# Kernel tuning notes

Hardware: AMD Instinct MI355X
Metric: run time of the kernel (lower is better)

Reference implementation:

```python
import jax, jax.numpy as jnp
import numpy as np

OUT_SIZE = 7          # pooled output resolution
SR = 2                # sampling_ratio (samples per bin side)
SCALES = (0.25, 0.125, 0.0625, 0.03125)   # FPN P2..P5 -> min_level=2, max_level=5
MIN_LEVEL, MAX_LEVEL = 2, 5
CANON_SIZE, CANON_LEVEL = 224.0, 4.0


def _roi_align(feat, boxes, bidx, scale):
    """ROIAlignV2 (aligned=True), fixed sampling_ratio.
    feat: [N,C,H,W]; boxes: [M,4] (x1,y1,x2,y2 in image coords); bidx: [M] int.
    Returns [M,C,OUT_SIZE,OUT_SIZE]."""
    N, C, H, W = feat.shape
    featT = jnp.transpose(feat, (0, 2, 3, 1))  # [N,H,W,C] for channel-last gathers
    # aligned=True: half-pixel offset
    x1 = boxes[:, 0] * scale - 0.5
    y1 = boxes[:, 1] * scale - 0.5
    x2 = boxes[:, 2] * scale - 0.5
    y2 = boxes[:, 3] * scale - 0.5
    bw = (x2 - x1) / OUT_SIZE
    bh = (y2 - y1) / OUT_SIZE
    # flattened per-bin sample offsets: for bin i, sample j -> i + (j+0.5)/SR
    k = jnp.arange(OUT_SIZE * SR)
    off = (k // SR).astype(feat.dtype) + ((k % SR).astype(feat.dtype) + 0.5) / SR  # [P]
    ys = y1[:, None] + off[None, :] * bh[:, None]  # [M,P]
    xs = x1[:, None] + off[None, :] * bw[:, None]  # [M,P]
    # validity (torchvision semantics: zero outside [-1, size])
    vy = (ys >= -1.0) & (ys <= H)
    vx = (xs >= -1.0) & (xs <= W)
    valid = vy[:, :, None] & vx[:, None, :]        # [M,P,P]
    y = jnp.clip(ys, 0.0, H - 1.0)
    x = jnp.clip(xs, 0.0, W - 1.0)
    y0 = jnp.floor(y).astype(jnp.int32)
    x0 = jnp.floor(x).astype(jnp.int32)
    y1i = jnp.minimum(y0 + 1, H - 1)
    x1i = jnp.minimum(x0 + 1, W - 1)
    ly = y - y0.astype(y.dtype)
    lx = x - x0.astype(x.dtype)
    hy, hx = 1.0 - ly, 1.0 - lx

    def gather(yi, xi):  # -> [M,P,P,C]
        return featT[bidx[:, None, None], yi[:, :, None], xi[:, None, :]]

    val = (hy[:, :, None] * hx[:, None, :])[..., None] * gather(y0, x0)
    val = val + (hy[:, :, None] * lx[:, None, :])[..., None] * gather(y0, x1i)
    val = val + (ly[:, :, None] * hx[:, None, :])[..., None] * gather(y1i, x0)
    val = val + (ly[:, :, None] * lx[:, None, :])[..., None] * gather(y1i, x1i)
    val = jnp.where(valid[..., None], val, 0.0)
    M = boxes.shape[0]
    # average SRxSR samples per bin
    val = val.reshape(M, OUT_SIZE, SR, OUT_SIZE, SR, C).mean(axis=(2, 4))
    return jnp.transpose(val, (0, 3, 1, 2))  # [M,C,7,7]


def _pool(feats, boxes):
    N, R, _ = boxes.shape
    b = boxes.reshape(-1, 4)                        # [M,4], M = N*R (pooler-format concat)
    bidx = jnp.repeat(jnp.arange(N), R)             # batch index column
    # assign_boxes_to_levels: log2 area bucketing
    sizes = jnp.sqrt(jnp.maximum((b[:, 2] - b[:, 0]) * (b[:, 3] - b[:, 1]), 0.0))
    lvl = jnp.floor(CANON_LEVEL + jnp.log2(sizes / CANON_SIZE + 1e-8))
    lvl = jnp.clip(lvl, MIN_LEVEL, MAX_LEVEL).astype(jnp.int32) - MIN_LEVEL  # [M] in [0,3]
    out = jnp.zeros((b.shape[0], feats[0].shape[1], OUT_SIZE, OUT_SIZE), feats[0].dtype)
    for l, (f, s) in enumerate(zip(feats, SCALES)):
        pooled = _roi_align(f, b, bidx, s)
        out = out + jnp.where((lvl == l)[:, None, None, None], pooled, 0.0)
    return out


def setup_inputs() -> dict:
    key = jax.random.key(0)
    ks = jax.random.split(key, 6)
    N, R, IMG = 2, 512, 1024.0
    shapes = [(2, 256, 256, 256), (2, 256, 128, 128), (2, 256, 64, 64), (2, 256, 32, 32)]
    feats = [jax.random.normal(ks[i], s, dtype=jnp.float32) for i, s in enumerate(shapes)]
    # box sizes log-uniform in [32, 800] px so all 4 levels get boxes
    wh = jnp.exp(jax.random.uniform(ks[4], (N, R, 2), minval=jnp.log(32.0), maxval=jnp.log(800.0)))
    cxy = jax.random.uniform(ks[5], (N, R, 2), minval=0.0, maxval=IMG)
    x1y1 = jnp.clip(cxy - wh / 2, 0.0, IMG)
    x2y2 = jnp.clip(cxy + wh / 2, 0.0, IMG)
    boxes = jnp.concatenate([x1y1, x2y2], axis=-1)  # [N,R,4]
    return {"feat0": feats[0], "feat1": feats[1], "feat2": feats[2], "feat3": feats[3], "boxes": boxes}


def reference(feat0, feat1, feat2, feat3, boxes):
    return _pool((feat0, feat1, feat2, feat3), boxes)
```

## Files before the change

kernel.cpp:

```cpp
#include <hip/hip_runtime.h>

#define OUT 7
#define CCH 256

__device__ __forceinline__ unsigned short f2bf(float f) {
    union { float f; unsigned int u; } v; v.f = f;
    unsigned int r = (v.u + 0x7FFFu + ((v.u >> 16) & 1u)) >> 16;
    return (unsigned short)r;
}
__device__ __forceinline__ float bf2f(unsigned short h) {
    union { unsigned int u; float f; } v; v.u = ((unsigned int)h) << 16;
    return v.f;
}

__global__ __launch_bounds__(256) void roi_pool_naive(
    const float* __restrict__ f0, const float* __restrict__ f1,
    const float* __restrict__ f2, const float* __restrict__ f3,
    const float* __restrict__ boxes, float* __restrict__ out,
    int M, int R)
{
    int idx = blockIdx.x * blockDim.x + threadIdx.x;
    int total = M * CCH * OUT * OUT;
    if (idx >= total) return;
    int pw = idx % OUT;
    int ph = (idx / OUT) % OUT;
    int c  = (idx / (OUT * OUT)) % CCH;
    int m  = idx / (OUT * OUT * CCH);
    int n  = m / R;
    const float bx1 = boxes[m * 4 + 0], by1 = boxes[m * 4 + 1];
    const float bx2 = boxes[m * 4 + 2], by2 = boxes[m * 4 + 3];
    float sz  = sqrtf(fmaxf((bx2 - bx1) * (by2 - by1), 0.0f));
    int lvl = (int)floorf(4.0f + log2f(sz / 224.0f + 1e-8f));
    lvl = min(max(lvl, 2), 5) - 2;
    const float* feat; int H, W; float scale;
    switch (lvl) {
        case 0:  feat = f0; H = 256; W = 256; scale = 0.25f;    break;
        case 1:  feat = f1; H = 128; W = 128; scale = 0.125f;   break;
        case 2:  feat = f2; H = 64;  W = 64;  scale = 0.0625f;  break;
        default: feat = f3; H = 32;  W = 32;  scale = 0.03125f; break;
    }
    const float* fp = feat + (size_t)(n * CCH + c) * (size_t)(H * W);
    float x1 = bx1 * scale - 0.5f, y1 = by1 * scale - 0.5f;
    float x2 = bx2 * scale - 0.5f, y2 = by2 * scale - 0.5f;
    float bw = (x2 - x1) * (1.0f / OUT), bh = (y2 - y1) * (1.0f / OUT);
    float acc = 0.0f;
    #pragma unroll
    for (int iy = 0; iy < 2; iy++) {
        float ys = y1 + ((float)ph + ((float)iy + 0.5f) * 0.5f) * bh;
        bool vy = (ys >= -1.0f) && (ys <= (float)H);
        float y = fminf(fmaxf(ys, 0.0f), (float)(H - 1));
        int y0 = (int)y;
        int y1i = min(y0 + 1, H - 1);
        float ly = y - (float)y0, hy = 1.0f - ly;
        #pragma unroll
        for (int ix = 0; ix < 2; ix++) {
            float xs = x1 + ((float)pw + ((float)ix + 0.5f) * 0.5f) * bw;
            bool vx = (xs >= -1.0f) && (xs <= (float)W);
            float x = fminf(fmaxf(xs, 0.0f), (float)(W - 1));
            int x0 = (int)x;
            int x1ii = min(x0 + 1, W - 1);
            float lx = x - (float)x0, hx = 1.0f - lx;
            if (vy && vx) {
                acc += hy * hx * fp[y0 * W + x0]  + hy * lx * fp[y0 * W + x1ii]
                     + ly * hx * fp[y1i * W + x0] + ly * lx * fp[y1i * W + x1ii];
            }
        }
    }
    out[idx] = acc * 0.25f;
}

__global__ __launch_bounds__(256) void transpose_bf16(
    const float* __restrict__ in, unsigned short* __restrict__ outp, int HW)
{
    __shared__ float tile[64][65];
    int hw0 = blockIdx.x * 64;
    int c0  = blockIdx.y * 64;
    int n   = blockIdx.z;
    int tx = threadIdx.x;
    int ty = threadIdx.y;

    const float4* in4 = (const float4*)(in + (size_t)n * CCH * HW);
    #pragma unroll
    for (int j = 0; j < 4; j++) {
        int c = c0 + ty + 16 * j;
        float4 v = in4[((size_t)c * HW + hw0) / 4 + tx];
        tile[ty + 16 * j][4 * tx + 0] = v.x;
        tile[ty + 16 * j][4 * tx + 1] = v.y;
        tile[ty + 16 * j][4 * tx + 2] = v.z;
        tile[ty + 16 * j][4 * tx + 3] = v.w;
    }
    __syncthreads();
    unsigned short* ob = outp + (size_t)n * HW * CCH;
    #pragma unroll
    for (int j = 0; j < 4; j++) {
        int hw = hw0 + ty + 16 * j;
        ushort4 u;
        u.x = f2bf(tile[4 * tx + 0][ty + 16 * j]);
        u.y = f2bf(tile[4 * tx + 1][ty + 16 * j]);
        u.z = f2bf(tile[4 * tx + 2][ty + 16 * j]);
        u.w = f2bf(tile[4 * tx + 3][ty + 16 * j]);
        ((ushort4*)(ob + (size_t)hw * CCH + c0))[tx] = u;
    }
}

__global__ __launch_bounds__(256) void roi_pool_cl(
    const unsigned short* __restrict__ t0, const unsigned short* __restrict__ t1,
    const unsigned short* __restrict__ t2, const unsigned short* __restrict__ t3,
    const float* __restrict__ boxes, float* __restrict__ out, int M, int R)
{
    int bx = blockIdx.x;
    int m, ph;
    if ((M & 7) == 0) {
        int q = bx / 56, rem = bx - q * 56;
        ph = rem >> 3;
        m  = q * 8 + (rem & 7);
    } else {
        m = bx / OUT; ph = bx % OUT;
    }
    int t = threadIdx.x;
    int n = m / R;

    const float bx1 = boxes[m * 4 + 0], by1 = boxes[m * 4 + 1];
    const float bx2 = boxes[m * 4 + 2], by2 = boxes[m * 4 + 3];
    float sz  = sqrtf(fmaxf((bx2 - bx1) * (by2 - by1), 0.0f));
    int lvl = (int)floorf(4.0f + log2f(sz / 224.0f + 1e-8f));
    lvl = min(max(lvl, 2), 5) - 2;

    const unsigned short* feat; int H, W; float scale;
    switch (lvl) {
        case 0:  feat = t0; H = 256; W = 256; scale = 0.25f;    break;
        case 1:  feat = t1; H = 128; W = 128; scale = 0.125f;   break;
        case 2:  feat = t2; H = 64;  W = 64;  scale = 0.0625f;  break;
        default: feat = t3; H = 32;  W = 32;  scale = 0.03125f; break;
    }
    const unsigned short* fb = feat + (size_t)n * H * W * CCH;

    float x1 = bx1 * scale - 0.5f, y1 = by1 * scale - 0.5f;
    float x2 = bx2 * scale - 0.5f, y2 = by2 * scale - 0.5f;
    float bw = (x2 - x1) * (1.0f / OUT), bh = (y2 - y1) * (1.0f / OUT);

    int   r0[2], r1[2];
    float lyv[2], hyv[2];
    bool  vyv[2];
    #pragma unroll
    for (int iy = 0; iy < 2; iy++) {
        float ys = y1 + ((float)ph + ((float)iy + 0.5f) * 0.5f) * bh;
        vyv[iy] = (ys >= -1.0f) && (ys <= (float)H);
        float y = fminf(fmaxf(ys, 0.0f), (float)(H - 1));
        int y0 = (int)y;
        int y1i = min(y0 + 1, H - 1);
        lyv[iy] = y - (float)y0;
        hyv[iy] = 1.0f - lyv[iy];
        r0[iy] = y0 * W * CCH;
        r1[iy] = y1i * W * CCH;
    }

    float acc[OUT];
    #pragma unroll
    for (int pw = 0; pw < OUT; pw++) {
        float a = 0.0f;
        #pragma unroll
        for (int ix = 0; ix < 2; ix++) {
            float xs = x1 + ((float)pw + ((float)ix + 0.5f) * 0.5f) * bw;
            bool vx = (xs >= -1.0f) && (xs <= (float)W);
            float x = fminf(fmaxf(xs, 0.0f), (float)(W - 1));
            int x0 = (int)x;
            int x1i = min(x0 + 1, W - 1);
            float lx = x - (float)x0;
            float hx = 1.0f - lx;
            int c0o = x0 * CCH;
            int c1o = x1i * CCH;
            #pragma unroll
            for (int iy = 0; iy < 2; iy++) {
                if (vyv[iy] && vx) {
                    const unsigned short* p00 = fb + __builtin_amdgcn_readfirstlane(r0[iy] + c0o);
                    const unsigned short* p01 = fb + __builtin_amdgcn_readfirstlane(r0[iy] + c1o);
                    const unsigned short* p10 = fb + __builtin_amdgcn_readfirstlane(r1[iy] + c0o);
                    const unsigned short* p11 = fb + __builtin_amdgcn_readfirstlane(r1[iy] + c1o);
                    float v00 = bf2f(p00[t]), v01 = bf2f(p01[t]);
                    float v10 = bf2f(p10[t]), v11 = bf2f(p11[t]);
                    a += hyv[iy] * (hx * v00 + lx * v01)
                       + lyv[iy] * (hx * v10 + lx * v11);
                }
            }
        }
        acc[pw] = a * 0.25f;
    }

    float* ob = out + (size_t)m * (CCH * OUT * OUT) + (size_t)t * (OUT * OUT) + ph * OUT;
    #pragma unroll
    for (int k = 0; k < OUT; k++) ob[k] = acc[k];
}

extern "C" void kernel_launch(void* const* d_in, const int* in_sizes, int n_in,
                              void* d_out, int out_size, void* d_ws, size_t ws_size,
                              hipStream_t stream) {
    const float* f0    = (const float*)d_in[0];
    const float* f1    = (const float*)d_in[1];
    const float* f2    = (const float*)d_in[2];
    const float* f3    = (const float*)d_in[3];
    const float* boxes = (const float*)d_in[4];
    float* out = (float*)d_out;

    int N = in_sizes[0] / (CCH * 256 * 256);
    int M = in_sizes[4] / 4;
    int R = M / N;

    size_t nshorts = (size_t)N * CCH * (65536 + 16384 + 4096 + 1024);
    if (ws_size >= nshorts * sizeof(unsigned short)) {
        unsigned short* t0 = (unsigned short*)d_ws;
        unsigned short* t1 = t0 + (size_t)N * CCH * 65536;
        unsigned short* t2 = t1 + (size_t)N * CCH * 16384;
        unsigned short* t3 = t2 + (size_t)N * CCH * 4096;
        dim3 blk(16, 16);
        transpose_bf16<<<dim3(65536 / 64, CCH / 64, N), blk, 0, stream>>>(f0, t0, 65536);
        transpose_bf16<<<dim3(16384 / 64, CCH / 64, N), blk, 0, stream>>>(f1, t1, 16384);
        transpose_bf16<<<dim3(4096  / 64, CCH / 64, N), blk, 0, stream>>>(f2, t2, 4096);
        transpose_bf16<<<dim3(1024  / 64, CCH / 64, N), blk, 0, stream>>>(f3, t3, 1024);
        roi_pool_cl<<<M * OUT, 256, 0, stream>>>(t0, t1, t2, t3, boxes, out, M, R);
    } else {
        int total = M * CCH * OUT * OUT;
        roi_pool_naive<<<(total + 255) / 256, 256, 0, stream>>>(f0, f1, f2, f3, boxes, out, M, R);
    }
}
```

Before: 312.3 us.

## Merge per-level transposes into one launch and pool one box per block

Combines the four per-level channel-last bf16 transpose kernels into a single launch that decodes level, channel tile and batch from a flat block index. The pooling kernel now assigns one block per box and loops over all seven output rows, instead of one block per box row. This cuts launch overhead and repeated per-box setup, but reduces the pooling grid sevenfold, which lowers parallelism and latency hiding.

Result: slower. 386.5 us (+23.8%).

```diff
diff --git a/kernel.cpp b/kernel.cpp
--- a/kernel.cpp
+++ b/kernel.cpp
@@ -69,15 +69,35 @@
     out[idx] = acc * 0.25f;
 }
 
-__global__ __launch_bounds__(256) void transpose_bf16(
-    const float* __restrict__ in, unsigned short* __restrict__ outp, int HW)
+__global__ __launch_bounds__(256) void transpose_all(
+    const float* __restrict__ f0, const float* __restrict__ f1,
+    const float* __restrict__ f2, const float* __restrict__ f3,
+    unsigned short* __restrict__ o0, unsigned short* __restrict__ o1,
+    unsigned short* __restrict__ o2, unsigned short* __restrict__ o3,
+    int N)
 {
     __shared__ float tile[64][65];
-    int hw0 = blockIdx.x * 64;
-    int c0  = blockIdx.y * 64;
-    int n   = blockIdx.z;
-    int tx = threadIdx.x;
-    int ty = threadIdx.y;
+
+    int rem = blockIdx.x;
+    const int nb0 = 4096 * N;
+    const int nb1 = 1024 * N;
+    const int nb2 = 256 * N;
+    const float* in; unsigned short* op; int HW, lshift;
+    if (rem < nb0)        { in = f0; op = o0; HW = 65536; lshift = 10; }
+    else { rem -= nb0;
+      if (rem < nb1)      { in = f1; op = o1; HW = 16384; lshift = 8;  }
+      else { rem -= nb1;
+        if (rem < nb2)    { in = f2; op = o2; HW = 4096;  lshift = 6;  }
+        else { rem -= nb2;  in = f3; op = o3; HW = 1024;  lshift = 4;  }
+      }
+    }
+    int hw0 = (rem & ((1 << lshift) - 1)) << 6;
+    int c0  = ((rem >> lshift) & 3) << 6;
+    int n   = rem >> (lshift + 2);
+
+    int tid = threadIdx.x;
+    int tx = tid & 15;
+    int ty = tid >> 4;
 
     const float4* in4 = (const float4*)(in + (size_t)n * CCH * HW);
     #pragma unroll
@@ -90,7 +110,7 @@
         tile[ty + 16 * j][4 * tx + 3] = v.w;
     }
     __syncthreads();
-    unsigned short* ob = outp + (size_t)n * HW * CCH;
+    unsigned short* ob = op + (size_t)n * HW * CCH;
     #pragma unroll
     for (int j = 0; j < 4; j++) {
         int hw = hw0 + ty + 16 * j;
@@ -103,20 +123,12 @@
     }
 }
 
-__global__ __launch_bounds__(256) void roi_pool_cl(
+__global__ __launch_bounds__(256) void roi_pool_box(
     const unsigned short* __restrict__ t0, const unsigned short* __restrict__ t1,
     const unsigned short* __restrict__ t2, const unsigned short* __restrict__ t3,
     const float* __restrict__ boxes, float* __restrict__ out, int M, int R)
 {
-    int bx = blockIdx.x;
-    int m, ph;
-    if ((M & 7) == 0) {
-        int q = bx / 56, rem = bx - q * 56;
-        ph = rem >> 3;
-        m  = q * 8 + (rem & 7);
-    } else {
-        m = bx / OUT; ph = bx % OUT;
-    }
+    int m = blockIdx.x;
     int t = threadIdx.x;
     int n = m / R;
 
@@ -139,57 +151,61 @@
     float x2 = bx2 * scale - 0.5f, y2 = by2 * scale - 0.5f;
     float bw = (x2 - x1) * (1.0f / OUT), bh = (y2 - y1) * (1.0f / OUT);
 
-    int   r0[2], r1[2];
-    float lyv[2], hyv[2];
-    bool  vyv[2];
-    #pragma unroll
-    for (int iy = 0; iy < 2; iy++) {
-        float ys = y1 + ((float)ph + ((float)iy + 0.5f) * 0.5f) * bh;
-        vyv[iy] = (ys >= -1.0f) && (ys <= (float)H);
-        float y = fminf(fmaxf(ys, 0.0f), (float)(H - 1));
-        int y0 = (int)y;
-        int y1i = min(y0 + 1, H - 1);
-        lyv[iy] = y - (float)y0;
-        hyv[iy] = 1.0f - lyv[iy];
-        r0[iy] = y0 * W * CCH;
-        r1[iy] = y1i * W * CCH;
-    }
-
-    float acc[OUT];
-    #pragma unroll
-    for (int pw = 0; pw < OUT; pw++) {
-        float a = 0.0f;
-        #pragma unroll
-        for (int ix = 0; ix < 2; ix++) {
-            float xs = x1 + ((float)pw + ((float)ix + 0.5f) * 0.5f) * bw;
-            bool vx = (xs >= -1.0f) && (xs <= (float)W);
-            float x = fminf(fmaxf(xs, 0.0f), (float)(W - 1));
-            int x0 = (int)x;
-            int x1i = min(x0 + 1, W - 1);
-            float lx = x - (float)x0;
-            float hx = 1.0f - lx;
-            int c0o = x0 * CCH;
-            int c1o = x1i * CCH;
+    float* obase = out + (size_t)m * (CCH * OUT * OUT) + (size_t)t * (OUT * OUT);
+
+    for (int ph = 0; ph < OUT; ph++) {
+        int   r0[2], r1[2];
+        float lyv[2], hyv[2];
+        bool  vyv[2];
+        #pragma unroll
+        for (int iy = 0; iy < 2; iy++) {
+            float ys = y1 + ((float)ph + ((float)iy + 0.5f) * 0.5f) * bh;
+            vyv[iy] = (ys >= -1.0f) && (ys <= (float)H);
+            float y = fminf(fmaxf(ys, 0.0f), (float)(H - 1));
+            int y0 = (int)y;
+            int y1i = min(y0 + 1, H - 1);
+            lyv[iy] = y - (float)y0;
+            hyv[iy] = 1.0f - lyv[iy];
+            r0[iy] = y0 * W * CCH;
+            r1[iy] = y1i * W * CCH;
+        }
+
+        float acc[OUT];
+        #pragma unroll
+        for (int pw = 0; pw < OUT; pw++) {
+            float a = 0.0f;
             #pragma unroll
-            for (int iy = 0; iy < 2; iy++) {
-                if (vyv[iy] && vx) {
-                    const unsigned short* p00 = fb + __builtin_amdgcn_readfirstlane(r0[iy] + c0o);
-                    const unsigned short* p01 = fb + __builtin_amdgcn_readfirstlane(r0[iy] + c1o);
-                    const unsigned short* p10 = fb + __builtin_amdgcn_readfirstlane(r1[iy] + c0o);
-                    const unsigned short* p11 = fb + __builtin_amdgcn_readfirstlane(r1[iy] + c1o);
-                    float v00 = bf2f(p00[t]), v01 = bf2f(p01[t]);
-                    float v10 = bf2f(p10[t]), v11 = bf2f(p11[t]);
-                    a += hyv[iy] * (hx * v00 + lx * v01)
-                       + lyv[iy] * (hx * v10 + lx * v11);
+            for (int ix = 0; ix < 2; ix++) {
+                float xs = x1 + ((float)pw + ((float)ix + 0.5f) * 0.5f) * bw;
+                bool vx = (xs >= -1.0f) && (xs <= (float)W);
+                float x = fminf(fmaxf(xs, 0.0f), (float)(W - 1));
+                int x0 = (int)x;
+                int x1i = min(x0 + 1, W - 1);
+                float lx = x - (float)x0;
+                float hx = 1.0f - lx;
+                int c0o = x0 * CCH;
+                int c1o = x1i * CCH;
+                #pragma unroll
+                for (int iy = 0; iy < 2; iy++) {
+                    if (vyv[iy] && vx) {
+                        const unsigned short* p00 = fb + __builtin_amdgcn_readfirstlane(r0[iy] + c0o);
+                        const unsigned short* p01 = fb + __builtin_amdgcn_readfirstlane(r0[iy] + c1o);
+                        const unsigned short* p10 = fb + __builtin_amdgcn_readfirstlane(r1[iy] + c0o);
+                        const unsigned short* p11 = fb + __builtin_amdgcn_readfirstlane(r1[iy] + c1o);
+                        float v00 = bf2f(p00[t]), v01 = bf2f(p01[t]);
+                        float v10 = bf2f(p10[t]), v11 = bf2f(p11[t]);
+                        a += hyv[iy] * (hx * v00 + lx * v01)
+                           + lyv[iy] * (hx * v10 + lx * v11);
+                    }
                 }
             }
+            acc[pw] = a * 0.25f;
         }
-        acc[pw] = a * 0.25f;
-    }
-
-    float* ob = out + (size_t)m * (CCH * OUT * OUT) + (size_t)t * (OUT * OUT) + ph * OUT;
-    #pragma unroll
-    for (int k = 0; k < OUT; k++) ob[k] = acc[k];
+
+        float* ob = obase + ph * OUT;
+        #pragma unroll
+        for (int k = 0; k < OUT; k++) ob[k] = acc[k];
+    }
 }
 
 extern "C" void kernel_launch(void* const* d_in, const int* in_sizes, int n_in,
@@ -212,12 +228,9 @@
         unsigned short* t1 = t0 + (size_t)N * CCH * 65536;
         unsigned short* t2 = t1 + (size_t)N * CCH * 16384;
         unsigned short* t3 = t2 + (size_t)N * CCH * 4096;
-        dim3 blk(16, 16);
-        transpose_bf16<<<dim3(65536 / 64, CCH / 64, N), blk, 0, stream>>>(f0, t0, 65536);
-        transpose_bf16<<<dim3(16384 / 64, CCH / 64, N), blk, 0, stream>>>(f1, t1, 16384);
-        transpose_bf16<<<dim3(4096  / 64, CCH / 64, N), blk, 0, stream>>>(f2, t2, 4096);
-        transpose_bf16<<<dim3(1024  / 64, CCH / 64, N), blk, 0, stream>>>(f3, t3, 1024);
-        roi_pool_cl<<<M * OUT, 256, 0, stream>>>(t0, t1, t2, t3, boxes, out, M, R);
+        int tblocks = (4096 + 1024 + 256 + 64) * N;
+        transpose_all<<<tblocks, 256, 0, stream>>>(f0, f1, f2, f3, t0, t1, t2, t3, N);
+        roi_pool_box<<<M, 256, 0, stream>>>(t0, t1, t2, t3, boxes, out, M, R);
     } else {
         int total = M * CCH * OUT * OUT;
         roi_pool_naive<<<(total + 255) / 256, 256, 0, stream>>>(f0, f1, f2, f3, boxes, out, M, R);
```
